# Optimization experiments

Measured on AMD Instinct MI355X. Metric: run time of the kernel, lower is better.

Reference implementation:

```python
import jax, jax.numpy as jnp
import numpy as np

EPS = 1e-5
NEG = -1e9

def _ln(x, g, b):
    m = x.mean(-1, keepdims=True)
    v = ((x - m) ** 2).mean(-1, keepdims=True)
    return (x - m) / jnp.sqrt(v + EPS) * g + b

def setup_inputs() -> dict:
    key = jax.random.key(0)
    ks = jax.random.split(key, 32)
    B, N, D, F, L = 2, 512, 128, 512, 3
    s = 0.05
    rn = lambda k, sh, sc=s: jax.random.normal(k, sh, jnp.float32) * sc
    inp = {
        'rel_matrix': rn(ks[0], (B, N, N, 2), 1.0),
        'pre_w': rn(ks[1], (2, D)), 'pre_b': rn(ks[2], (D,)),
        'proj_w': rn(ks[3], (2 * D, D)), 'proj_b': rn(ks[4], (D,)),
        'out_w1': rn(ks[5], (D, D)),
        'bn_g': 1.0 + rn(ks[6], (D,)), 'bn_b': rn(ks[7], (D,)),
        'bn_m': rn(ks[8], (D,)),
        'bn_v': 0.5 + jax.random.uniform(ks[9], (D,), jnp.float32),
        'out_w2': rn(ks[10], (D, D)), 'out_b2': rn(ks[11], (D,)),
        'pe': rn(ks[12], (128, D)),
        'wq': rn(ks[13], (L, D, D)), 'bq': rn(ks[14], (L, D)),
        'wk': rn(ks[15], (L, D, D)), 'bk': rn(ks[16], (L, D)),
        'wv': rn(ks[17], (L, D, D)), 'bv': rn(ks[18], (L, D)),
        'wo': rn(ks[19], (L, D, D)), 'bo': rn(ks[20], (L, D)),
        'ln1g': jnp.ones((L, D), jnp.float32), 'ln1b': jnp.zeros((L, D), jnp.float32),
        'ln2g': jnp.ones((L, D), jnp.float32), 'ln2b': jnp.zeros((L, D), jnp.float32),
        'fw1': rn(ks[21], (L, D, F)), 'fb1': rn(ks[22], (L, F)),
        'fw2': rn(ks[23], (L, F, D)), 'fb2': rn(ks[24], (L, D)),
        'mask': jax.random.randint(ks[25], (B, N), 0, 2) > 0,
        'agent_id': jax.random.randint(ks[26], (B, N), 0, 128, dtype=jnp.int32),
    }
    return inp

def reference(rel_matrix, pre_w, pre_b, proj_w, proj_b, out_w1, bn_g, bn_b, bn_m, bn_v,
              out_w2, out_b2, pe, wq, bq, wk, bk, wv, bv, wo, bo,
              ln1g, ln1b, ln2g, ln2b, fw1, fb1, fw2, fb2, mask, agent_id):
    # --- pairwise relation chain (the headroom target) ---
    # symmetric pairwise validity mask (B,N,N)
    pm = (mask[:, None, :] & mask[:, :, None]).astype(rel_matrix.dtype)
    count = jnp.maximum(pm.sum(axis=2), 1.0)  # (B,N) valid-partner counts
    x = rel_matrix @ pre_w + pre_b            # (B,N,N,D) pre_proj Linear(2->128)
    pooled = jnp.einsum('bijd,bij->bid', x, pm) / count[..., None]  # masked mean over j
    x = jnp.concatenate([x, jnp.broadcast_to(pooled[:, :, None, :], x.shape)], axis=-1)
    x = x @ proj_w + proj_b                   # Linear(256->128)
    x = jnp.einsum('bijd,bij->bid', x, pm) / count[..., None]       # masked mean over j
    # out MLP: Linear(no bias) + BatchNorm1d(eval) + ReLU + Linear
    h = x @ out_w1
    h = (h - bn_m) / jnp.sqrt(bn_v + EPS) * bn_g + bn_b
    x = jax.nn.relu(h) @ out_w2 + out_b2
    x = x + pe[agent_id]                      # agent positional embedding
    # --- 3 post-norm single-head transformer layers (eval, dropout off) ---
    kbias = jnp.where(mask, 0.0, NEG)[:, None, :]  # key padding bias (B,1,N)
    scale = 1.0 / jnp.sqrt(jnp.asarray(x.shape[-1], x.dtype))
    for l in range(3):
        q = x @ wq[l] + bq[l]
        k = x @ wk[l] + bk[l]
        v = x @ wv[l] + bv[l]
        a = jax.nn.softmax(jnp.einsum('bid,bjd->bij', q, k) * scale + kbias, axis=-1)
        att = jnp.einsum('bij,bjd->bid', a, v) @ wo[l] + bo[l]
        x = _ln(x + att, ln1g[l], ln1b[l])
        ff = jax.nn.relu(x @ fw1[l] + fb1[l]) @ fw2[l] + fb2[l]
        x = _ln(x + ff, ln2g[l], ln2b[l])
    return x
```

## Files before the change

### kernel.cpp

```cpp
#include <hip/hip_runtime.h>
#include <hip/hip_bf16.h>

typedef unsigned short u16;
typedef unsigned int u32;
typedef unsigned char u8;
typedef __attribute__((ext_vector_type(8))) short bf16x8;
typedef __attribute__((ext_vector_type(4))) float f32x4;

#define DEV __device__ __forceinline__

DEV float bf2f(u16 u) { union { u32 i; float f; } c; c.i = ((u32)u) << 16; return c.f; }
DEV u16 f2bf(float f) {
  union { float f; u32 i; } c; c.f = f;
  u32 r = c.i + 0x7FFFu + ((c.i >> 16) & 1u);
  return (u16)(r >> 16);
}
DEV u32 pk2(float lo, float hi) { return (u32)f2bf(lo) | ((u32)f2bf(hi) << 16); }
DEV float rdsrc(const void* p, int e, int isb) {
  return isb ? bf2f(((const u16*)p)[e]) : ((const float*)p)[e];
}
DEV bf16x8 as_bf(uint4 v) { union { uint4 u; bf16x8 h; } c; c.u = v; return c.h; }

static constexpr int B = 2, N = 512, D = 128, F = 512;
static constexpr int NROW = B * N;
static constexpr float EPS = 1e-5f;
static constexpr float NEG = -1e9f;
static constexpr float SCALE = 0.08838834764831845f;

#define OFF_PRE_W   0
#define OFF_PRE_B   256
#define OFF_PROJ_B  33152
#define OFF_BN_G    49664
#define OFF_BN_B    49792
#define OFF_BN_M    49920
#define OFF_BN_V    50048
#define OFF_OUT_B2  66560
#define OFF_PE      66688
#define OFF_BQ      132224
#define OFF_BK      181760
#define OFF_BV      231296
#define OFF_BO      280832
#define OFF_LN1G    281216
#define OFF_LN1B    281600
#define OFF_LN2G    281984
#define OFF_LN2B    282368
#define OFF_FB1     479360
#define OFF_FB2     677504
#define W_TOTAL     677888

static constexpr int PB_PROJ = 0;
static constexpr int PB_OW1  = 8192;
static constexpr int PB_OW2  = 16384;
static constexpr int PB_L0   = 24576;
static constexpr int PB_LSTR = 98304;
static constexpr int PB_WO   = 24576;
static constexpr int PB_FW1  = 32768;
static constexpr int PB_FW2  = 65536;
static constexpr int PTOT    = 79872;

struct NEnt { const void* s; int off, n; };
struct PEnt { const void* s1; const void* s2; int o1, o2, dst, lgn, cum; };
struct PrepArgs { NEnt nrm[19]; PEnt pk[21]; };

template<int KT>
DEV f32x4 mmaK(const uint4* __restrict__ aPk, const uint4* __restrict__ Bp,
               int ncol, int col, int lane) {
  f32x4 acc = {0.f, 0.f, 0.f, 0.f};
  const int sub = lane >> 4;
  #pragma unroll
  for (int kt = 0; kt < KT; ++kt) {
    const int e8 = kt * 4 + sub;
    acc = __builtin_amdgcn_mfma_f32_16x16x32_bf16(
        as_bf(aPk[e8 * 16 + (lane & 15)]),
        as_bf(Bp[(size_t)e8 * ncol + col]),
        acc, 0, 0, 0);
  }
  return acc;
}

DEV void packA(const float* __restrict__ src, int ld, int K,
               uint4* __restrict__ aPk, int t) {
  const int n = (K >> 3) * 4;
  for (int i = t; i < n; i += 512) {
    const int e8 = i >> 2, r = i & 3;
    const float* s = src + r * ld + e8 * 8;
    uint4 w;
    w.x = pk2(s[0], s[1]); w.y = pk2(s[2], s[3]);
    w.z = pk2(s[4], s[5]); w.w = pk2(s[6], s[7]);
    aPk[e8 * 16 + r] = w;
  }
}

__global__ __launch_bounds__(256) void k_prep(PrepArgs pa,
    const void* __restrict__ bnv, const void* __restrict__ maskp,
    int* __restrict__ flags, int* __restrict__ mbuf,
    float* __restrict__ W, u32* __restrict__ Wb)
{
  const int t = threadIdx.x, bid = blockIdx.x;
  __shared__ int s_nb, s_m4, s_m2;
  if (t == 0) { s_nb = 0; s_m4 = 0; s_m2 = 0; }
  __syncthreads();
  if (t < 64) {
    const u32 w = ((const u32*)bnv)[t];
    if (((w >> 8) & 0xFFu) != 0x3Fu || ((w >> 24) & 0xFFu) != 0x3Fu)
      atomicOr(&s_nb, 1);
  }
  __syncthreads();
  const int isb = s_nb ? 0 : 1;

  if (bid < 16) {
    for (int ten = 0; ten < 19; ++ten) {
      const NEnt E = pa.nrm[ten];
      for (int e = bid * 256 + t; e < E.n; e += 16 * 256)
        W[E.off + e] = rdsrc(E.s, e, isb);
    }
  } else if (bid < 143) {
    for (int g = (bid - 16) * 256 + t; g < PTOT; g += 127 * 256) {
      int ei = 0;
      #pragma unroll
      for (int k = 1; k < 21; ++k) if (g >= pa.pk[k].cum) ei = k;
      const PEnt E = pa.pk[ei];
      const int li = g - E.cum;
      const int e8 = li >> E.lgn, c = li & ((1 << E.lgn) - 1);
      float f[8];
      #pragma unroll
      for (int i = 0; i < 8; ++i) {
        const int si = ((e8 * 8 + i) << E.lgn) + c;
        f[i] = rdsrc(E.s1, E.o1 + si, isb);
        if (E.s2) f[i] += rdsrc(E.s2, E.o2 + si, isb);
      }
      uint4 w;
      w.x = pk2(f[0], f[1]); w.y = pk2(f[2], f[3]);
      w.z = pk2(f[4], f[5]); w.w = pk2(f[6], f[7]);
      ((uint4*)(Wb + E.dst))[li] = w;
    }
  } else {
    {
      const u32 w = ((const u32*)maskp)[t];
      if (!(w == 0u || w == 1u || w == 0x3F800000u)) atomicOr(&s_m4, 1);
      if (!(w == 0u || w == 1u || w == 0x10000u || w == 0x10001u ||
            w == 0x3F80u || w == 0x3F800000u || w == 0x3F803F80u)) atomicOr(&s_m2, 1);
    }
    __syncthreads();
    const int mode = (!s_m4) ? 4 : ((!s_m2) ? 2 : 1);
    if (t == 0) { flags[0] = isb; flags[1] = mode; }
    #pragma unroll
    for (int k = 0; k < 4; ++k) {
      const int e = k * 256 + t;
      int v;
      if (mode == 4)      v = (((const u32*)maskp)[e] != 0u);
      else if (mode == 2) v = (((const u16*)maskp)[e] != 0);
      else                v = (((const u8*)maskp)[e]  != 0);
      mbuf[e] = v;
    }
  }
}

__global__ __launch_bounds__(512) void k_relq(
    const void* __restrict__ relv, const float* __restrict__ W,
    const u32* __restrict__ Wb,
    const int* __restrict__ flags, const int* __restrict__ mbuf,
    const int* __restrict__ agent_id, float* __restrict__ xbuf,
    float* __restrict__ qb, u32* __restrict__ kbT, u32* __restrict__ vbT)
{
  const int t = threadIdx.x;
  const int row0 = blockIdx.x * 4;
  const int b = row0 >> 9;
  const int wid = t >> 6;
  const int lane = t & 63;

  __shared__ float pl[4][D], zl[4][D], rl[4][D], os[4][D];
  __shared__ float pA[4][D], pB[4][D];
  __shared__ uint4 aPk[1024];
  __shared__ float wred[8][9];
  __shared__ float sT0[4], sT1[4], sMt;

  float s0[4] = {0, 0, 0, 0}, s1[4] = {0, 0, 0, 0}, cnt;
  {
    const int j = t;
    const float m = (float)mbuf[b * N + j];
    cnt = m;
    if (flags[0]) {
      const u32* rel2 = (const u32*)relv;
      #pragma unroll
      for (int r = 0; r < 4; ++r) {
        const u32 u = rel2[(size_t)(row0 + r) * N + j];
        s0[r] += m * bf2f((u16)(u & 0xFFFFu));
        s1[r] += m * bf2f((u16)(u >> 16));
      }
    } else {
      const float2* relf = (const float2*)relv;
      #pragma unroll
      for (int r = 0; r < 4; ++r) {
        const float2 u = relf[(size_t)(row0 + r) * N + j];
        s0[r] += m * u.x; s1[r] += m * u.y;
      }
    }
  }
  {
    const uint4 z = {0u, 0u, 0u, 0u};
    aPk[t] = z; aPk[t + 512] = z;
  }
  #pragma unroll
  for (int o = 32; o > 0; o >>= 1) {
    #pragma unroll
    for (int r = 0; r < 4; ++r) {
      s0[r] += __shfl_xor(s0[r], o, 64);
      s1[r] += __shfl_xor(s1[r], o, 64);
    }
    cnt += __shfl_xor(cnt, o, 64);
  }
  if ((t & 63) == 0) {
    #pragma unroll
    for (int r = 0; r < 4; ++r) { wred[wid][r] = s0[r]; wred[wid][4 + r] = s1[r]; }
    wred[wid][8] = cnt;
  }
  __syncthreads();
  if (t < 4) {
    float a0 = 0, a1 = 0;
    #pragma unroll
    for (int w = 0; w < 8; ++w) { a0 += wred[w][t]; a1 += wred[w][4 + t]; }
    sT0[t] = a0; sT1[t] = a1;
  }
  if (t == 8) {
    float c = 0;
    #pragma unroll
    for (int w = 0; w < 8; ++w) c += wred[w][8];
    sMt = c;
  }
  __syncthreads();

  {
    const int r = t >> 7, c = t & 127;
    const int mi = mbuf[row0 + r];
    pl[r][c] = mi ? (sT0[r] * W[OFF_PRE_W + c] + sT1[r] * W[OFF_PRE_W + D + c]) / sMt
                    + W[OFF_PRE_B + c]
                  : 0.f;
  }
  __syncthreads();

  packA(&pl[0][0], D, D, aPk, t);
  __syncthreads();
  {
    const int col = wid * 16 + (lane & 15);
    f32x4 acc = mmaK<4>(aPk, (const uint4*)(Wb + PB_PROJ), 128, col, lane);
    if (lane < 16) {
      #pragma unroll
      for (int g = 0; g < 4; ++g) pA[g][col] = acc[g];
    }
  }
  __syncthreads();
  {
    const int r = t >> 7, d = t & 127;
    zl[r][d] = mbuf[row0 + r] ? pA[r][d] + W[OFF_PROJ_B + d] : 0.f;
  }
  __syncthreads();

  packA(&zl[0][0], D, D, aPk, t);
  __syncthreads();
  {
    const int col = wid * 16 + (lane & 15);
    f32x4 acc = mmaK<4>(aPk, (const uint4*)(Wb + PB_OW1), 128, col, lane);
    if (lane < 16) {
      #pragma unroll
      for (int g = 0; g < 4; ++g) pA[g][col] = acc[g];
    }
  }
  __syncthreads();
  {
    const int r = t >> 7, d = t & 127;
    const float hb = (pA[r][d] - W[OFF_BN_M + d]) * __frsqrt_rn(W[OFF_BN_V + d] + EPS)
                     * W[OFF_BN_G + d] + W[OFF_BN_B + d];
    rl[r][d] = fmaxf(hb, 0.f);
  }
  __syncthreads();

  packA(&rl[0][0], D, D, aPk, t);
  __syncthreads();
  {
    const int col = wid * 16 + (lane & 15);
    f32x4 acc = mmaK<4>(aPk, (const uint4*)(Wb + PB_OW2), 128, col, lane);
    if (lane < 16) {
      #pragma unroll
      for (int g = 0; g < 4; ++g) pA[g][col] = acc[g];
    }
  }
  __syncthreads();
  {
    const int r = t >> 7, d = t & 127;
    const int aid = agent_id[row0 + r];
    const float x0 = pA[r][d] + W[OFF_OUT_B2 + d] + W[OFF_PE + aid * D + d];
    os[r][d] = x0;
    xbuf[(size_t)(row0 + r) * D + d] = x0;
  }
  __syncthreads();

  packA(&os[0][0], D, D, aPk, t);
  __syncthreads();
  {
    const int col = wid * 16 + (lane & 15);
    #pragma unroll
    for (int m = 0; m < 3; ++m) {
      f32x4 acc = mmaK<4>(aPk, (const uint4*)(Wb + PB_L0 + m * 8192), 128, col, lane);
      if (lane < 16) {
        const float bb = W[(m == 0 ? OFF_BQ : m == 1 ? OFF_BK : OFF_BV) + col];
        if (m == 0) {
          #pragma unroll
          for (int g = 0; g < 4; ++g) qb[(size_t)(row0 + g) * D + col] = acc[g] + bb;
        } else if (m == 1) {
          #pragma unroll
          for (int g = 0; g < 4; ++g) pA[g][col] = acc[g] + bb;
        } else {
          #pragma unroll
          for (int g = 0; g < 4; ++g) pB[g][col] = acc[g] + bb;
        }
      }
    }
  }
  __syncthreads();
  if (t < 64) {
    const int r = t >> 4, e8 = t & 15;
    const float* ks = pA[r];
    uint4 w;
    w.x = pk2(ks[8 * e8 + 0], ks[8 * e8 + 1]);
    w.y = pk2(ks[8 * e8 + 2], ks[8 * e8 + 3]);
    w.z = pk2(ks[8 * e8 + 4], ks[8 * e8 + 5]);
    w.w = pk2(ks[8 * e8 + 6], ks[8 * e8 + 7]);
    ((uint4*)kbT)[((size_t)b * 16 + e8) * 512 + (row0 & 511) + r] = w;
  }
  if (t < 128) {
    const int i0 = row0 & 511, j8 = i0 >> 3, h = (i0 >> 2) & 1;
    uint2 w;
    w.x = pk2(pB[0][t], pB[1][t]);
    w.y = pk2(pB[2][t], pB[3][t]);
    *(uint2*)(vbT + (((size_t)b * 64 + j8) * 128 + t) * 4 + 2 * h) = w;
  }
}

__global__ __launch_bounds__(512) void k_layer(
    const float* __restrict__ qin, const u32* __restrict__ kinT, const u32* __restrict__ vinT,
    const float* __restrict__ W, const u32* __restrict__ Wb, const int l, const int last,
    float* __restrict__ qout, u32* __restrict__ koutT, u32* __restrict__ voutT,
    const int* __restrict__ mbuf, float* __restrict__ xbuf, float* __restrict__ outp)
{
  const int t = threadIdx.x;
  const int row0 = blockIdx.x * 4;
  const int b = row0 >> 9;
  const int wid = t >> 6;
  const int lane = t & 63;

  const uint4* WOp = (const uint4*)(Wb + PB_L0 + l * PB_LSTR + PB_WO);
  const uint4* W1p = (const uint4*)(Wb + PB_L0 + l * PB_LSTR + PB_FW1);
  const uint4* W2p = (const uint4*)(Wb + PB_L0 + l * PB_LSTR + PB_FW2);
  const float* bo  = W + OFF_BO  + l * D;
  const float* g1  = W + OFF_LN1G + l * D;
  const float* b1  = W + OFF_LN1B + l * D;
  const float* fb1 = W + OFF_FB1 + l * F;
  const float* fb2 = W + OFF_FB2 + l * D;
  const float* g2  = W + OFF_LN2G + l * D;
  const float* b2v = W + OFF_LN2B + l * D;

  __shared__ float qs[4][D];
  __shared__ float p[4][N];
  __shared__ float hs[4][F];
  __shared__ float os[4][D];
  __shared__ float xs[4][D];
  __shared__ float pA[4][D], pB[4][D];
  __shared__ uint4 aPk[1024];
  __shared__ float den[4];

  {
    const int r = t >> 7, d = t & 127;
    qs[r][d] = qin[(size_t)(row0 + r) * D + d] * SCALE;
    const uint4 z = {0u, 0u, 0u, 0u};
    aPk[t] = z; aPk[t + 512] = z;
  }
  __syncthreads();

  packA(&qs[0][0], D, D, aPk, t);
  __syncthreads();
  {
    const uint4* Kp = (const uint4*)kinT + (size_t)b * 16 * 512;
    #pragma unroll
    for (int i = 0; i < 4; ++i) {
      const int col = (wid * 4 + i) * 16 + (lane & 15);
      f32x4 acc = mmaK<4>(aPk, Kp, 512, col, lane);
      if (lane < 16) {
        const float bias = mbuf[b * N + col] ? 0.f : NEG;
        #pragma unroll
        for (int g = 0; g < 4; ++g) p[g][col] = acc[g] + bias;
      }
    }
  }
  __syncthreads();

  if (wid < 4) {
    const int r = wid;
    float pv[8];
    float mx = -1e30f;
    #pragma unroll
    for (int k = 0; k < 8; ++k) { pv[k] = p[r][lane + 64 * k]; mx = fmaxf(mx, pv[k]); }
    #pragma unroll
    for (int o = 32; o > 0; o >>= 1) mx = fmaxf(mx, __shfl_xor(mx, o, 64));
    float sum = 0.f;
    #pragma unroll
    for (int k = 0; k < 8; ++k) { pv[k] = __expf(pv[k] - mx); sum += pv[k]; }
    #pragma unroll
    for (int o = 32; o > 0; o >>= 1) sum += __shfl_xor(sum, o, 64);
    #pragma unroll
    for (int k = 0; k < 8; ++k) p[r][lane + 64 * k] = pv[k];
    if (lane == 0) den[r] = sum;
  }
  __syncthreads();

  packA(&p[0][0], N, N, aPk, t);
  __syncthreads();
  {
    const int col = wid * 16 + (lane & 15);
    const uint4* Vp = (const uint4*)vinT + (size_t)b * 64 * 128;
    f32x4 acc = mmaK<16>(aPk, Vp, 128, col, lane);
    if (lane < 16) {
      #pragma unroll
      for (int g = 0; g < 4; ++g) os[g][col] = acc[g] / den[g];
    }
  }
  __syncthreads();

  packA(&os[0][0], D, D, aPk, t);
  __syncthreads();
  {
    const int col = wid * 16 + (lane & 15);
    f32x4 acc = mmaK<4>(aPk, WOp, 128, col, lane);
    if (lane < 16) {
      #pragma unroll
      for (int g = 0; g < 4; ++g) pA[g][col] = acc[g];
    }
  }
  __syncthreads();

  if (wid < 4) {
    const int r = wid;
    float tv[2];
    #pragma unroll
    for (int k = 0; k < 2; ++k) {
      const int d = lane + 64 * k;
      tv[k] = pA[r][d] + bo[d] + xbuf[(size_t)(row0 + r) * D + d];
    }
    float s = tv[0] + tv[1], sq = tv[0] * tv[0] + tv[1] * tv[1];
    #pragma unroll
    for (int o = 32; o > 0; o >>= 1) { s += __shfl_xor(s, o, 64); sq += __shfl_xor(sq, o, 64); }
    const float mean = s * (1.f / 128.f);
    const float var  = sq * (1.f / 128.f) - mean * mean;
    const float rstd = __frsqrt_rn(var + EPS);
    #pragma unroll
    for (int k = 0; k < 2; ++k) {
      const int d = lane + 64 * k;
      xs[r][d] = (tv[k] - mean) * rstd * g1[d] + b1[d];
    }
  }
  __syncthreads();

  packA(&xs[0][0], D, D, aPk, t);
  __syncthreads();
  {
    #pragma unroll
    for (int i = 0; i < 4; ++i) {
      const int col = (wid * 4 + i) * 16 + (lane & 15);
      f32x4 acc = mmaK<4>(aPk, W1p, 512, col, lane);
      if (lane < 16) {
        const float bb = fb1[col];
        #pragma unroll
        for (int g = 0; g < 4; ++g) hs[g][col] = fmaxf(acc[g] + bb, 0.f);
      }
    }
  }
  __syncthreads();

  packA(&hs[0][0], F, F, aPk, t);
  __syncthreads();
  {
    const int col = wid * 16 + (lane & 15);
    f32x4 acc = mmaK<16>(aPk, W2p, 128, col, lane);
    if (lane < 16) {
      #pragma unroll
      for (int g = 0; g < 4; ++g) pA[g][col] = acc[g];
    }
  }
  __syncthreads();

  if (wid < 4) {
    const int r = wid;
    float tv[2];
    #pragma unroll
    for (int k = 0; k < 2; ++k) {
      const int d = lane + 64 * k;
      tv[k] = pA[r][d] + fb2[d] + xs[r][d];
    }
    float s = tv[0] + tv[1], sq = tv[0] * tv[0] + tv[1] * tv[1];
    #pragma unroll
    for (int o = 32; o > 0; o >>= 1) { s += __shfl_xor(s, o, 64); sq += __shfl_xor(sq, o, 64); }
    const float mean = s * (1.f / 128.f);
    const float var  = sq * (1.f / 128.f) - mean * mean;
    const float rstd = __frsqrt_rn(var + EPS);
    #pragma unroll
    for (int k = 0; k < 2; ++k) {
      const int d = lane + 64 * k;
      const float xn = (tv[k] - mean) * rstd * g2[d] + b2v[d];
      os[r][d] = xn;
      xbuf[(size_t)(row0 + r) * D + d] = xn;
      if (outp) outp[(size_t)(row0 + r) * D + d] = xn;
    }
  }
  __syncthreads();

  if (!last) {
    packA(&os[0][0], D, D, aPk, t);
    __syncthreads();
    {
      const int col = wid * 16 + (lane & 15);
      #pragma unroll
      for (int m = 0; m < 3; ++m) {
        const uint4* Bp = (const uint4*)(Wb + PB_L0 + (l + 1) * PB_LSTR + m * 8192);
        f32x4 acc = mmaK<4>(aPk, Bp, 128, col, lane);
        if (lane < 16) {
          const float bb = W[(m == 0 ? OFF_BQ : m == 1 ? OFF_BK : OFF_BV) + (l + 1) * D + col];
          if (m == 0) {
            #pragma unroll
            for (int g = 0; g < 4; ++g) qout[(size_t)(row0 + g) * D + col] = acc[g] + bb;
          } else if (m == 1) {
            #pragma unroll
            for (int g = 0; g < 4; ++g) pA[g][col] = acc[g] + bb;
          } else {
            #pragma unroll
            for (int g = 0; g < 4; ++g) pB[g][col] = acc[g] + bb;
          }
        }
      }
    }
    __syncthreads();
    if (t < 64) {
      const int r = t >> 4, e8 = t & 15;
      const float* ks = pA[r];
      uint4 w;
      w.x = pk2(ks[8 * e8 + 0], ks[8 * e8 + 1]);
      w.y = pk2(ks[8 * e8 + 2], ks[8 * e8 + 3]);
      w.z = pk2(ks[8 * e8 + 4], ks[8 * e8 + 5]);
      w.w = pk2(ks[8 * e8 + 6], ks[8 * e8 + 7]);
      ((uint4*)koutT)[((size_t)b * 16 + e8) * 512 + (row0 & 511) + r] = w;
    }
    if (t < 128) {
      const int i0 = row0 & 511, j8 = i0 >> 3, h = (i0 >> 2) & 1;
      uint2 w;
      w.x = pk2(pB[0][t], pB[1][t]);
      w.y = pk2(pB[2][t], pB[3][t]);
      *(uint2*)(voutT + (((size_t)b * 64 + j8) * 128 + t) * 4 + 2 * h) = w;
    }
  }
}

extern "C" void kernel_launch(void* const* d_in, const int* in_sizes, int n_in,
                              void* d_out, int out_size, void* d_ws, size_t ws_size,
                              hipStream_t stream) {
  int*   flags = (int*)d_ws;
  int*   mbuf  = flags + 16;
  float* xbuf  = (float*)d_ws + 1040;
  float* q0    = xbuf + NROW * D;
  float* q1    = q0 + NROW * D;
  u32*   kT0   = (u32*)(q1 + NROW * D);
  u32*   kT1   = kT0 + 65536;
  u32*   vT0   = kT1 + 65536;
  u32*   vT1   = vT0 + 65536;
  float* W     = (float*)(vT1 + 65536);
  u32*   Wb    = (u32*)(W + W_TOTAL);

  PrepArgs pa;
  {
    const NEnt nrm[19] = {
      {d_in[1],  OFF_PRE_W,  256}, {d_in[2],  OFF_PRE_B, 128},
      {d_in[4],  OFF_PROJ_B, 128},
      {d_in[6],  OFF_BN_G,   128}, {d_in[7],  OFF_BN_B,  128},
      {d_in[8],  OFF_BN_M,   128}, {d_in[9],  OFF_BN_V,  128},
      {d_in[11], OFF_OUT_B2, 128}, {d_in[12], OFF_PE,  16384},
      {d_in[14], OFF_BQ,     384}, {d_in[16], OFF_BK,    384},
      {d_in[18], OFF_BV,     384}, {d_in[20], OFF_BO,    384},
      {d_in[21], OFF_LN1G,   384}, {d_in[22], OFF_LN1B,  384},
      {d_in[23], OFF_LN2G,   384}, {d_in[24], OFF_LN2B,  384},
      {d_in[26], OFF_FB1,   1536}, {d_in[28], OFF_FB2,   384}};
    for (int i = 0; i < 19; ++i) pa.nrm[i] = nrm[i];

    pa.pk[0] = {d_in[3], d_in[3], 0, 16384, PB_PROJ, 7, 0};
    pa.pk[1] = {d_in[5],  nullptr, 0, 0, PB_OW1, 7, 2048};
    pa.pk[2] = {d_in[10], nullptr, 0, 0, PB_OW2, 7, 4096};
    for (int l = 0; l < 3; ++l) {
      const int lb = PB_L0 + l * PB_LSTR;
      const int cl = 6144 + l * 24576;
      pa.pk[3 + 6 * l + 0] = {d_in[13], nullptr, l * 16384, 0, lb,          7, cl};
      pa.pk[3 + 6 * l + 1] = {d_in[15], nullptr, l * 16384, 0, lb + 8192,   7, cl + 2048};
      pa.pk[3 + 6 * l + 2] = {d_in[17], nullptr, l * 16384, 0, lb + 16384,  7, cl + 4096};
      pa.pk[3 + 6 * l + 3] = {d_in[19], nullptr, l * 16384, 0, lb + PB_WO,  7, cl + 6144};
      pa.pk[3 + 6 * l + 4] = {d_in[25], nullptr, l * 65536, 0, lb + PB_FW1, 9, cl + 8192};
      pa.pk[3 + 6 * l + 5] = {d_in[27], nullptr, l * 65536, 0, lb + PB_FW2, 7, cl + 16384};
    }
  }
  const int* agent_id = (const int*)d_in[30];

  k_prep<<<144, 256, 0, stream>>>(pa, d_in[9], d_in[29], flags, mbuf, W, Wb);
  k_relq<<<NROW / 4, 512, 0, stream>>>(d_in[0], W, Wb, flags, mbuf, agent_id, xbuf,
                                       q0, kT0, vT0);

  float* qs_[2] = {q0, q1};
  u32*   ks_[2] = {kT0, kT1};
  u32*   vs_[2] = {vT0, vT1};
  for (int l = 0; l < 3; ++l) {
    const int cur = l & 1, nxt = cur ^ 1;
    const int last = (l == 2);
    k_layer<<<NROW / 4, 512, 0, stream>>>(
        qs_[cur], ks_[cur], vs_[cur],
        W, Wb, l, last,
        qs_[nxt], ks_[nxt], vs_[nxt],
        mbuf, xbuf, last ? (float*)d_out : (float*)nullptr);
  }
}
```

Before: 77.32 us.

## Fuse prep, relation and layer kernels into one persistent kernel with grid barriers

Replaces five separate kernel launches (prep, relation chain, three transformer layers) with a single 256-block persistent kernel. Stages are separated by atomic-counter grid barriers, and a memset resets the counters on each call. This removes launch gaps and inter-kernel drain between stages. In exchange it relies on all 256 blocks being co-resident, adds spin-wait barrier cost, and spreads the prep work over the same blocks.

```diff
diff --git a/kernel.cpp b/kernel.cpp
--- a/kernel.cpp
+++ b/kernel.cpp
@@ -62,6 +62,18 @@
 struct PEnt { const void* s1; const void* s2; int o1, o2, dst, lgn, cum; };
 struct PrepArgs { NEnt nrm[19]; PEnt pk[21]; };
 
+DEV void gsync(int* c, int nblk) {
+  __syncthreads();
+  if (threadIdx.x == 0) {
+    __threadfence();
+    __hip_atomic_fetch_add(c, 1, __ATOMIC_ACQ_REL, __HIP_MEMORY_SCOPE_AGENT);
+    while (__hip_atomic_load(c, __ATOMIC_ACQUIRE, __HIP_MEMORY_SCOPE_AGENT) < nblk)
+      __builtin_amdgcn_s_sleep(8);
+    __threadfence();
+  }
+  __syncthreads();
+}
+
 template<int KT>
 DEV f32x4 mmaK(const uint4* __restrict__ aPk, const uint4* __restrict__ Bp,
                int ncol, int col, int lane) {
@@ -91,13 +103,30 @@
   }
 }
 
-__global__ __launch_bounds__(256) void k_prep(PrepArgs pa,
-    const void* __restrict__ bnv, const void* __restrict__ maskp,
-    int* __restrict__ flags, int* __restrict__ mbuf,
-    float* __restrict__ W, u32* __restrict__ Wb)
+__global__ __launch_bounds__(512) void k_all(PrepArgs pa,
+    const void* __restrict__ relv, const void* __restrict__ bnv,
+    const void* __restrict__ maskp, const int* __restrict__ agent_id,
+    int* __restrict__ bar, int* __restrict__ mbuf,
+    float* __restrict__ xbuf, float* __restrict__ q0, float* __restrict__ q1,
+    u32* __restrict__ kT0, u32* __restrict__ kT1,
+    u32* __restrict__ vT0, u32* __restrict__ vT1,
+    float* __restrict__ W, u32* __restrict__ Wb, float* __restrict__ outp)
 {
-  const int t = threadIdx.x, bid = blockIdx.x;
+  const int t = threadIdx.x;
+  const int blk = blockIdx.x;
+  const int row0 = blk * 4;
+  const int b = row0 >> 9;
+  const int wid = t >> 6;
+  const int lane = t & 63;
+
+  __shared__ float bufA[4][512];
+  __shared__ float r0[4][128], r1[4][128], r2[4][128], r3[4][128], r4[4][128];
+  __shared__ uint4 aPk[1024];
+  __shared__ float wred[8][9];
+  __shared__ float sT0[4], sT1[4];
+  __shared__ float sMt, den[4];
   __shared__ int s_nb, s_m4, s_m2;
+
   if (t == 0) { s_nb = 0; s_m4 = 0; s_m2 = 0; }
   __syncthreads();
   if (t < 64) {
@@ -108,34 +137,32 @@
   __syncthreads();
   const int isb = s_nb ? 0 : 1;
 
-  if (bid < 16) {
-    for (int ten = 0; ten < 19; ++ten) {
-      const NEnt E = pa.nrm[ten];
-      for (int e = bid * 256 + t; e < E.n; e += 16 * 256)
-        W[E.off + e] = rdsrc(E.s, e, isb);
-    }
-  } else if (bid < 143) {
-    for (int g = (bid - 16) * 256 + t; g < PTOT; g += 127 * 256) {
-      int ei = 0;
-      #pragma unroll
-      for (int k = 1; k < 21; ++k) if (g >= pa.pk[k].cum) ei = k;
-      const PEnt E = pa.pk[ei];
-      const int li = g - E.cum;
-      const int e8 = li >> E.lgn, c = li & ((1 << E.lgn) - 1);
-      float f[8];
-      #pragma unroll
-      for (int i = 0; i < 8; ++i) {
-        const int si = ((e8 * 8 + i) << E.lgn) + c;
-        f[i] = rdsrc(E.s1, E.o1 + si, isb);
-        if (E.s2) f[i] += rdsrc(E.s2, E.o2 + si, isb);
-      }
-      uint4 w;
-      w.x = pk2(f[0], f[1]); w.y = pk2(f[2], f[3]);
-      w.z = pk2(f[4], f[5]); w.w = pk2(f[6], f[7]);
-      ((uint4*)(Wb + E.dst))[li] = w;
-    }
-  } else {
-    {
+  for (int ten = 0; ten < 19; ++ten) {
+    const NEnt E = pa.nrm[ten];
+    for (int e = blk * 512 + t; e < E.n; e += 256 * 512)
+      W[E.off + e] = rdsrc(E.s, e, isb);
+  }
+  for (int g = blk * 512 + t; g < PTOT; g += 256 * 512) {
+    int ei = 0;
+    #pragma unroll
+    for (int k = 1; k < 21; ++k) if (g >= pa.pk[k].cum) ei = k;
+    const PEnt E = pa.pk[ei];
+    const int li = g - E.cum;
+    const int e8 = li >> E.lgn, c = li & ((1 << E.lgn) - 1);
+    float f[8];
+    #pragma unroll
+    for (int i = 0; i < 8; ++i) {
+      const int si = ((e8 * 8 + i) << E.lgn) + c;
+      f[i] = rdsrc(E.s1, E.o1 + si, isb);
+      if (E.s2) f[i] += rdsrc(E.s2, E.o2 + si, isb);
+    }
+    uint4 w;
+    w.x = pk2(f[0], f[1]); w.y = pk2(f[2], f[3]);
+    w.z = pk2(f[4], f[5]); w.w = pk2(f[6], f[7]);
+    ((uint4*)(Wb + E.dst))[li] = w;
+  }
+  if (blk == 255) {
+    if (t < 256) {
       const u32 w = ((const u32*)maskp)[t];
       if (!(w == 0u || w == 1u || w == 0x3F800000u)) atomicOr(&s_m4, 1);
       if (!(w == 0u || w == 1u || w == 0x10000u || w == 0x10001u ||
@@ -143,10 +170,9 @@
     }
     __syncthreads();
     const int mode = (!s_m4) ? 4 : ((!s_m2) ? 2 : 1);
-    if (t == 0) { flags[0] = isb; flags[1] = mode; }
     #pragma unroll
-    for (int k = 0; k < 4; ++k) {
-      const int e = k * 256 + t;
+    for (int k = 0; k < 2; ++k) {
+      const int e = k * 512 + t;
       int v;
       if (mode == 4)      v = (((const u32*)maskp)[e] != 0u);
       else if (mode == 2) v = (((const u16*)maskp)[e] != 0);
@@ -154,385 +180,147 @@
       mbuf[e] = v;
     }
   }
-}
-
-__global__ __launch_bounds__(512) void k_relq(
-    const void* __restrict__ relv, const float* __restrict__ W,
-    const u32* __restrict__ Wb,
-    const int* __restrict__ flags, const int* __restrict__ mbuf,
-    const int* __restrict__ agent_id, float* __restrict__ xbuf,
-    float* __restrict__ qb, u32* __restrict__ kbT, u32* __restrict__ vbT)
-{
-  const int t = threadIdx.x;
-  const int row0 = blockIdx.x * 4;
-  const int b = row0 >> 9;
-  const int wid = t >> 6;
-  const int lane = t & 63;
-
-  __shared__ float pl[4][D], zl[4][D], rl[4][D], os[4][D];
-  __shared__ float pA[4][D], pB[4][D];
-  __shared__ uint4 aPk[1024];
-  __shared__ float wred[8][9];
-  __shared__ float sT0[4], sT1[4], sMt;
-
-  float s0[4] = {0, 0, 0, 0}, s1[4] = {0, 0, 0, 0}, cnt;
+  gsync(bar + 0, 256);
+
   {
-    const int j = t;
-    const float m = (float)mbuf[b * N + j];
-    cnt = m;
-    if (flags[0]) {
-      const u32* rel2 = (const u32*)relv;
+    float s0[4] = {0, 0, 0, 0}, s1[4] = {0, 0, 0, 0}, cnt;
+    {
+      const int j = t;
+      const float m = (float)mbuf[b * N + j];
+      cnt = m;
+      if (isb) {
+        const u32* rel2 = (const u32*)relv;
+        #pragma unroll
+        for (int r = 0; r < 4; ++r) {
+          const u32 u = rel2[(size_t)(row0 + r) * N + j];
+          s0[r] += m * bf2f((u16)(u & 0xFFFFu));
+          s1[r] += m * bf2f((u16)(u >> 16));
+        }
+      } else {
+        const float2* relf = (const float2*)relv;
+        #pragma unroll
+        for (int r = 0; r < 4; ++r) {
+          const float2 u = relf[(size_t)(row0 + r) * N + j];
+          s0[r] += m * u.x; s1[r] += m * u.y;
+        }
+      }
+    }
+    {
+      const uint4 z = {0u, 0u, 0u, 0u};
+      aPk[t] = z; aPk[t + 512] = z;
+    }
+    #pragma unroll
+    for (int o = 32; o > 0; o >>= 1) {
       #pragma unroll
       for (int r = 0; r < 4; ++r) {
-        const u32 u = rel2[(size_t)(row0 + r) * N + j];
-        s0[r] += m * bf2f((u16)(u & 0xFFFFu));
-        s1[r] += m * bf2f((u16)(u >> 16));
-      }
-    } else {
-      const float2* relf = (const float2*)relv;
-      #pragma unroll
-      for (int r = 0; r < 4; ++r) {
-        const float2 u = relf[(size_t)(row0 + r) * N + j];
-        s0[r] += m * u.x; s1[r] += m * u.y;
-      }
-    }
-  }
-  {
-    const uint4 z = {0u, 0u, 0u, 0u};
-    aPk[t] = z; aPk[t + 512] = z;
-  }
-  #pragma unroll
-  for (int o = 32; o > 0; o >>= 1) {
-    #pragma unroll
-    for (int r = 0; r < 4; ++r) {
-      s0[r] += __shfl_xor(s0[r], o, 64);
-      s1[r] += __shfl_xor(s1[r], o, 64);
-    }
-    cnt += __shfl_xor(cnt, o, 64);
-  }
-  if ((t & 63) == 0) {
-    #pragma unroll
-    for (int r = 0; r < 4; ++r) { wred[wid][r] = s0[r]; wred[wid][4 + r] = s1[r]; }
-    wred[wid][8] = cnt;
-  }
-  __syncthreads();
-  if (t < 4) {
-    float a0 = 0, a1 = 0;
-    #pragma unroll
-    for (int w = 0; w < 8; ++w) { a0 += wred[w][t]; a1 += wred[w][4 + t]; }
-    sT0[t] = a0; sT1[t] = a1;
-  }
-  if (t == 8) {
-    float c = 0;
-    #pragma unroll
-    for (int w = 0; w < 8; ++w) c += wred[w][8];
-    sMt = c;
-  }
-  __syncthreads();
-
-  {
-    const int r = t >> 7, c = t & 127;
-    const int mi = mbuf[row0 + r];
-    pl[r][c] = mi ? (sT0[r] * W[OFF_PRE_W + c] + sT1[r] * W[OFF_PRE_W + D + c]) / sMt
-                    + W[OFF_PRE_B + c]
-                  : 0.f;
-  }
-  __syncthreads();
-
-  packA(&pl[0][0], D, D, aPk, t);
-  __syncthreads();
-  {
-    const int col = wid * 16 + (lane & 15);
-    f32x4 acc = mmaK<4>(aPk, (const uint4*)(Wb + PB_PROJ), 128, col, lane);
-    if (lane < 16) {
-      #pragma unroll
-      for (int g = 0; g < 4; ++g) pA[g][col] = acc[g];
-    }
-  }
-  __syncthreads();
-  {
-    const int r = t >> 7, d = t & 127;
-    zl[r][d] = mbuf[row0 + r] ? pA[r][d] + W[OFF_PROJ_B + d] : 0.f;
-  }
-  __syncthreads();
-
-  packA(&zl[0][0], D, D, aPk, t);
-  __syncthreads();
-  {
-    const int col = wid * 16 + (lane & 15);
-    f32x4 acc = mmaK<4>(aPk, (const uint4*)(Wb + PB_OW1), 128, col, lane);
-    if (lane < 16) {
-      #pragma unroll
-      for (int g = 0; g < 4; ++g) pA[g][col] = acc[g];
-    }
-  }
-  __syncthreads();
-  {
-    const int r = t >> 7, d = t & 127;
-    const float hb = (pA[r][d] - W[OFF_BN_M + d]) * __frsqrt_rn(W[OFF_BN_V + d] + EPS)
-                     * W[OFF_BN_G + d] + W[OFF_BN_B + d];
-    rl[r][d] = fmaxf(hb, 0.f);
-  }
-  __syncthreads();
-
-  packA(&rl[0][0], D, D, aPk, t);
-  __syncthreads();
-  {
-    const int col = wid * 16 + (lane & 15);
-    f32x4 acc = mmaK<4>(aPk, (const uint4*)(Wb + PB_OW2), 128, col, lane);
-    if (lane < 16) {
-      #pragma unroll
-      for (int g = 0; g < 4; ++g) pA[g][col] = acc[g];
-    }
-  }
-  __syncthreads();
-  {
-    const int r = t >> 7, d = t & 127;
-    const int aid = agent_id[row0 + r];
-    const float x0 = pA[r][d] + W[OFF_OUT_B2 + d] + W[OFF_PE + aid * D + d];
-    os[r][d] = x0;
-    xbuf[(size_t)(row0 + r) * D + d] = x0;
-  }
-  __syncthreads();
-
-  packA(&os[0][0], D, D, aPk, t);
-  __syncthreads();
-  {
-    const int col = wid * 16 + (lane & 15);
-    #pragma unroll
-    for (int m = 0; m < 3; ++m) {
-      f32x4 acc = mmaK<4>(aPk, (const uint4*)(Wb + PB_L0 + m * 8192), 128, col, lane);
+        s0[r] += __shfl_xor(s0[r], o, 64);
+        s1[r] += __shfl_xor(s1[r], o, 64);
+      }
+      cnt += __shfl_xor(cnt, o, 64);
+    }
+    if ((t & 63) == 0) {
+      #pragma unroll
+      for (int r = 0; r < 4; ++r) { wred[wid][r] = s0[r]; wred[wid][4 + r] = s1[r]; }
+      wred[wid][8] = cnt;
+    }
+    __syncthreads();
+    if (t < 4) {
+      float a0 = 0, a1 = 0;
+      #pragma unroll
+      for (int w = 0; w < 8; ++w) { a0 += wred[w][t]; a1 += wred[w][4 + t]; }
+      sT0[t] = a0; sT1[t] = a1;
+    }
+    if (t == 8) {
+      float c = 0;
+      #pragma unroll
+      for (int w = 0; w < 8; ++w) c += wred[w][8];
+      sMt = c;
+    }
+    __syncthreads();
+
+    {
+      const int r = t >> 7, c = t & 127;
+      const int mi = mbuf[row0 + r];
+      r0[r][c] = mi ? (sT0[r] * W[OFF_PRE_W + c] + sT1[r] * W[OFF_PRE_W + D + c]) / sMt
+                      + W[OFF_PRE_B + c]
+                    : 0.f;
+    }
+    __syncthreads();
+
+    packA(&r0[0][0], D, D, aPk, t);
+    __syncthreads();
+    {
+      const int col = wid * 16 + (lane & 15);
+      f32x4 acc = mmaK<4>(aPk, (const uint4*)(Wb + PB_PROJ), 128, col, lane);
       if (lane < 16) {
-        const float bb = W[(m == 0 ? OFF_BQ : m == 1 ? OFF_BK : OFF_BV) + col];
-        if (m == 0) {
-          #pragma unroll
-          for (int g = 0; g < 4; ++g) qb[(size_t)(row0 + g) * D + col] = acc[g] + bb;
-        } else if (m == 1) {
-          #pragma unroll
-          for (int g = 0; g < 4; ++g) pA[g][col] = acc[g] + bb;
-        } else {
-          #pragma unroll
-          for (int g = 0; g < 4; ++g) pB[g][col] = acc[g] + bb;
-        }
-      }
-    }
-  }
-  __syncthreads();
-  if (t < 64) {
-    const int r = t >> 4, e8 = t & 15;
-    const float* ks = pA[r];
-    uint4 w;
-    w.x = pk2(ks[8 * e8 + 0], ks[8 * e8 + 1]);
-    w.y = pk2(ks[8 * e8 + 2], ks[8 * e8 + 3]);
-    w.z = pk2(ks[8 * e8 + 4], ks[8 * e8 + 5]);
-    w.w = pk2(ks[8 * e8 + 6], ks[8 * e8 + 7]);
-    ((uint4*)kbT)[((size_t)b * 16 + e8) * 512 + (row0 & 511) + r] = w;
-  }
-  if (t < 128) {
-    const int i0 = row0 & 511, j8 = i0 >> 3, h = (i0 >> 2) & 1;
-    uint2 w;
-    w.x = pk2(pB[0][t], pB[1][t]);
-    w.y = pk2(pB[2][t], pB[3][t]);
-    *(uint2*)(vbT + (((size_t)b * 64 + j8) * 128 + t) * 4 + 2 * h) = w;
-  }
-}
-
-__global__ __launch_bounds__(512) void k_layer(
-    const float* __restrict__ qin, const u32* __restrict__ kinT, const u32* __restrict__ vinT,
-    const float* __restrict__ W, const u32* __restrict__ Wb, const int l, const int last,
-    float* __restrict__ qout, u32* __restrict__ koutT, u32* __restrict__ voutT,
-    const int* __restrict__ mbuf, float* __restrict__ xbuf, float* __restrict__ outp)
-{
-  const int t = threadIdx.x;
-  const int row0 = blockIdx.x * 4;
-  const int b = row0 >> 9;
-  const int wid = t >> 6;
-  const int lane = t & 63;
-
-  const uint4* WOp = (const uint4*)(Wb + PB_L0 + l * PB_LSTR + PB_WO);
-  const uint4* W1p = (const uint4*)(Wb + PB_L0 + l * PB_LSTR + PB_FW1);
-  const uint4* W2p = (const uint4*)(Wb + PB_L0 + l * PB_LSTR + PB_FW2);
-  const float* bo  = W + OFF_BO  + l * D;
-  const float* g1  = W + OFF_LN1G + l * D;
-  const float* b1  = W + OFF_LN1B + l * D;
-  const float* fb1 = W + OFF_FB1 + l * F;
-  const float* fb2 = W + OFF_FB2 + l * D;
-  const float* g2  = W + OFF_LN2G + l * D;
-  const float* b2v = W + OFF_LN2B + l * D;
-
-  __shared__ float qs[4][D];
-  __shared__ float p[4][N];
-  __shared__ float hs[4][F];
-  __shared__ float os[4][D];
-  __shared__ float xs[4][D];
-  __shared__ float pA[4][D], pB[4][D];
-  __shared__ uint4 aPk[1024];
-  __shared__ float den[4];
-
-  {
-    const int r = t >> 7, d = t & 127;
-    qs[r][d] = qin[(size_t)(row0 + r) * D + d] * SCALE;
-    const uint4 z = {0u, 0u, 0u, 0u};
-    aPk[t] = z; aPk[t + 512] = z;
-  }
-  __syncthreads();
-
-  packA(&qs[0][0], D, D, aPk, t);
-  __syncthreads();
-  {
-    const uint4* Kp = (const uint4*)kinT + (size_t)b * 16 * 512;
-    #pragma unroll
-    for (int i = 0; i < 4; ++i) {
-      const int col = (wid * 4 + i) * 16 + (lane & 15);
-      f32x4 acc = mmaK<4>(aPk, Kp, 512, col, lane);
+        #pragma unroll
+        for (int g = 0; g < 4; ++g) r4[g][col] = acc[g];
+      }
+    }
+    __syncthreads();
+    {
+      const int r = t >> 7, d = t & 127;
+      r1[r][d] = mbuf[row0 + r] ? r4[r][d] + W[OFF_PROJ_B + d] : 0.f;
+    }
+    __syncthreads();
+
+    packA(&r1[0][0], D, D, aPk, t);
+    __syncthreads();
+    {
+      const int col = wid * 16 + (lane & 15);
+      f32x4 acc = mmaK<4>(aPk, (const uint4*)(Wb + PB_OW1), 128, col, lane);
       if (lane < 16) {
-        const float bias = mbuf[b * N + col] ? 0.f : NEG;
-        #pragma unroll
-        for (int g = 0; g < 4; ++g) p[g][col] = acc[g] + bias;
-      }
-    }
-  }
-  __syncthreads();
-
-  if (wid < 4) {
-    const int r = wid;
-    float pv[8];
-    float mx = -1e30f;
-    #pragma unroll
-    for (int k = 0; k < 8; ++k) { pv[k] = p[r][lane + 64 * k]; mx = fmaxf(mx, pv[k]); }
-    #pragma unroll
-    for (int o = 32; o > 0; o >>= 1) mx = fmaxf(mx, __shfl_xor(mx, o, 64));
-    float sum = 0.f;
-    #pragma unroll
-    for (int k = 0; k < 8; ++k) { pv[k] = __expf(pv[k] - mx); sum += pv[k]; }
-    #pragma unroll
-    for (int o = 32; o > 0; o >>= 1) sum += __shfl_xor(sum, o, 64);
-    #pragma unroll
-    for (int k = 0; k < 8; ++k) p[r][lane + 64 * k] = pv[k];
-    if (lane == 0) den[r] = sum;
-  }
-  __syncthreads();
-
-  packA(&p[0][0], N, N, aPk, t);
-  __syncthreads();
-  {
-    const int col = wid * 16 + (lane & 15);
-    const uint4* Vp = (const uint4*)vinT + (size_t)b * 64 * 128;
-    f32x4 acc = mmaK<16>(aPk, Vp, 128, col, lane);
-    if (lane < 16) {
-      #pragma unroll
-      for (int g = 0; g < 4; ++g) os[g][col] = acc[g] / den[g];
-    }
-  }
-  __syncthreads();
-
-  packA(&os[0][0], D, D, aPk, t);
-  __syncthreads();
-  {
-    const int col = wid * 16 + (lane & 15);
-    f32x4 acc = mmaK<4>(aPk, WOp, 128, col, lane);
-    if (lane < 16) {
-      #pragma unroll
-      for (int g = 0; g < 4; ++g) pA[g][col] = acc[g];
-    }
-  }
-  __syncthreads();
-
-  if (wid < 4) {
-    const int r = wid;
-    float tv[2];
-    #pragma unroll
-    for (int k = 0; k < 2; ++k) {
-      const int d = lane + 64 * k;
-      tv[k] = pA[r][d] + bo[d] + xbuf[(size_t)(row0 + r) * D + d];
-    }
-    float s = tv[0] + tv[1], sq = tv[0] * tv[0] + tv[1] * tv[1];
-    #pragma unroll
-    for (int o = 32; o > 0; o >>= 1) { s += __shfl_xor(s, o, 64); sq += __shfl_xor(sq, o, 64); }
-    const float mean = s * (1.f / 128.f);
-    const float var  = sq * (1.f / 128.f) - mean * mean;
-    const float rstd = __frsqrt_rn(var + EPS);
-    #pragma unroll
-    for (int k = 0; k < 2; ++k) {
-      const int d = lane + 64 * k;
-      xs[r][d] = (tv[k] - mean) * rstd * g1[d] + b1[d];
-    }
-  }
-  __syncthreads();
-
-  packA(&xs[0][0], D, D, aPk, t);
-  __syncthreads();
-  {
-    #pragma unroll
-    for (int i = 0; i < 4; ++i) {
-      const int col = (wid * 4 + i) * 16 + (lane & 15);
-      f32x4 acc = mmaK<4>(aPk, W1p, 512, col, lane);
+        #pragma unroll
+        for (int g = 0; g < 4; ++g) r4[g][col] = acc[g];
+      }
+    }
+    __syncthreads();
+    {
+      const int r = t >> 7, d = t & 127;
+      const float hb = (r4[r][d] - W[OFF_BN_M + d]) * __frsqrt_rn(W[OFF_BN_V + d] + EPS)
+                       * W[OFF_BN_G + d] + W[OFF_BN_B + d];
+      r2[r][d] = fmaxf(hb, 0.f);
+    }
+    __syncthreads();
+
+    packA(&r2[0][0], D, D, aPk, t);
+    __syncthreads();
+    {
+      const int col = wid * 16 + (lane & 15);
+      f32x4 acc = mmaK<4>(aPk, (const uint4*)(Wb + PB_OW2), 128, col, lane);
       if (lane < 16) {
-        const float bb = fb1[col];
-        #pragma unroll
-        for (int g = 0; g < 4; ++g) hs[g][col] = fmaxf(acc[g] + bb, 0.f);
-      }
-    }
-  }
-  __syncthreads();
-
-  packA(&hs[0][0], F, F, aPk, t);
-  __syncthreads();
-  {
-    const int col = wid * 16 + (lane & 15);
-    f32x4 acc = mmaK<16>(aPk, W2p, 128, col, lane);
-    if (lane < 16) {
-      #pragma unroll
-      for (int g = 0; g < 4; ++g) pA[g][col] = acc[g];
-    }
-  }
-  __syncthreads();
-
-  if (wid < 4) {
-    const int r = wid;
-    float tv[2];
-    #pragma unroll
-    for (int k = 0; k < 2; ++k) {
-      const int d = lane + 64 * k;
-      tv[k] = pA[r][d] + fb2[d] + xs[r][d];
-    }
-    float s = tv[0] + tv[1], sq = tv[0] * tv[0] + tv[1] * tv[1];
-    #pragma unroll
-    for (int o = 32; o > 0; o >>= 1) { s += __shfl_xor(s, o, 64); sq += __shfl_xor(sq, o, 64); }
-    const float mean = s * (1.f / 128.f);
-    const float var  = sq * (1.f / 128.f) - mean * mean;
-    const float rstd = __frsqrt_rn(var + EPS);
-    #pragma unroll
-    for (int k = 0; k < 2; ++k) {
-      const int d = lane + 64 * k;
-      const float xn = (tv[k] - mean) * rstd * g2[d] + b2v[d];
-      os[r][d] = xn;
-      xbuf[(size_t)(row0 + r) * D + d] = xn;
-      if (outp) outp[(size_t)(row0 + r) * D + d] = xn;
-    }
-  }
-  __syncthreads();
-
-  if (!last) {
-    packA(&os[0][0], D, D, aPk, t);
+        #pragma unroll
+        for (int g = 0; g < 4; ++g) r4[g][col] = acc[g];
+      }
+    }
+    __syncthreads();
+    {
+      const int r = t >> 7, d = t & 127;
+      const int aid = agent_id[row0 + r];
+      const float x0 = r4[r][d] + W[OFF_OUT_B2 + d] + W[OFF_PE + aid * D + d];
+      r3[r][d] = x0;
+      xbuf[(size_t)(row0 + r) * D + d] = x0;
+    }
+    __syncthreads();
+
+    packA(&r3[0][0], D, D, aPk, t);
     __syncthreads();
     {
       const int col = wid * 16 + (lane & 15);
       #pragma unroll
       for (int m = 0; m < 3; ++m) {
-        const uint4* Bp = (const uint4*)(Wb + PB_L0 + (l + 1) * PB_LSTR + m * 8192);
-        f32x4 acc = mmaK<4>(aPk, Bp, 128, col, lane);
+        f32x4 acc = mmaK<4>(aPk, (const uint4*)(Wb + PB_L0 + m * 8192), 128, col, lane);
         if (lane < 16) {
-          const float bb = W[(m == 0 ? OFF_BQ : m == 1 ? OFF_BK : OFF_BV) + (l + 1) * D + col];
+          const float bb = W[(m == 0 ? OFF_BQ : m == 1 ? OFF_BK : OFF_BV) + col];
           if (m == 0) {
             #pragma unroll
-            for (int g = 0; g < 4; ++g) qout[(size_t)(row0 + g) * D + col] = acc[g] + bb;
+            for (int g = 0; g < 4; ++g) q0[(size_t)(row0 + g) * D + col] = acc[g] + bb;
           } else if (m == 1) {
             #pragma unroll
-            for (int g = 0; g < 4; ++g) pA[g][col] = acc[g] + bb;
+            for (int g = 0; g < 4; ++g) r4[g][col] = acc[g] + bb;
           } else {
             #pragma unroll
-            for (int g = 0; g < 4; ++g) pB[g][col] = acc[g] + bb;
+            for (int g = 0; g < 4; ++g) bufA[g][col] = acc[g] + bb;
           }
         }
       }
@@ -540,20 +328,229 @@
     __syncthreads();
     if (t < 64) {
       const int r = t >> 4, e8 = t & 15;
-      const float* ks = pA[r];
+      const float* ks = r4[r];
       uint4 w;
       w.x = pk2(ks[8 * e8 + 0], ks[8 * e8 + 1]);
       w.y = pk2(ks[8 * e8 + 2], ks[8 * e8 + 3]);
       w.z = pk2(ks[8 * e8 + 4], ks[8 * e8 + 5]);
       w.w = pk2(ks[8 * e8 + 6], ks[8 * e8 + 7]);
-      ((uint4*)koutT)[((size_t)b * 16 + e8) * 512 + (row0 & 511) + r] = w;
+      ((uint4*)kT0)[((size_t)b * 16 + e8) * 512 + (row0 & 511) + r] = w;
     }
     if (t < 128) {
       const int i0 = row0 & 511, j8 = i0 >> 3, h = (i0 >> 2) & 1;
       uint2 w;
-      w.x = pk2(pB[0][t], pB[1][t]);
-      w.y = pk2(pB[2][t], pB[3][t]);
-      *(uint2*)(voutT + (((size_t)b * 64 + j8) * 128 + t) * 4 + 2 * h) = w;
+      w.x = pk2(bufA[0][t], bufA[1][t]);
+      w.y = pk2(bufA[2][t], bufA[3][t]);
+      *(uint2*)(vT0 + (((size_t)b * 64 + j8) * 128 + t) * 4 + 2 * h) = w;
+    }
+  }
+  gsync(bar + 1, 256);
+
+  for (int l = 0; l < 3; ++l) {
+    const int last = (l == 2);
+    const float* qin = (l & 1) ? q1 : q0;
+    float*       qout = (l & 1) ? q0 : q1;
+    const u32*   kin = (l & 1) ? kT1 : kT0;
+    u32*         kout = (l & 1) ? kT0 : kT1;
+    const u32*   vin = (l & 1) ? vT1 : vT0;
+    u32*         vout = (l & 1) ? vT0 : vT1;
+
+    const uint4* WOp = (const uint4*)(Wb + PB_L0 + l * PB_LSTR + PB_WO);
+    const uint4* W1p = (const uint4*)(Wb + PB_L0 + l * PB_LSTR + PB_FW1);
+    const uint4* W2p = (const uint4*)(Wb + PB_L0 + l * PB_LSTR + PB_FW2);
+    const float* bo  = W + OFF_BO  + l * D;
+    const float* g1  = W + OFF_LN1G + l * D;
+    const float* b1  = W + OFF_LN1B + l * D;
+    const float* fb1 = W + OFF_FB1 + l * F;
+    const float* fb2 = W + OFF_FB2 + l * D;
+    const float* g2  = W + OFF_LN2G + l * D;
+    const float* b2v = W + OFF_LN2B + l * D;
+
+    {
+      const int r = t >> 7, d = t & 127;
+      r0[r][d] = qin[(size_t)(row0 + r) * D + d] * SCALE;
+    }
+    __syncthreads();
+
+    packA(&r0[0][0], D, D, aPk, t);
+    __syncthreads();
+    {
+      const uint4* Kp = (const uint4*)kin + (size_t)b * 16 * 512;
+      #pragma unroll
+      for (int i = 0; i < 4; ++i) {
+        const int col = (wid * 4 + i) * 16 + (lane & 15);
+        f32x4 acc = mmaK<4>(aPk, Kp, 512, col, lane);
+        if (lane < 16) {
+          const float bias = mbuf[b * N + col] ? 0.f : NEG;
+          #pragma unroll
+          for (int g = 0; g < 4; ++g) bufA[g][col] = acc[g] + bias;
+        }
+      }
+    }
+    __syncthreads();
+
+    if (wid < 4) {
+      const int r = wid;
+      float pv[8];
+      float mx = -1e30f;
+      #pragma unroll
+      for (int k = 0; k < 8; ++k) { pv[k] = bufA[r][lane + 64 * k]; mx = fmaxf(mx, pv[k]); }
+      #pragma unroll
+      for (int o = 32; o > 0; o >>= 1) mx = fmaxf(mx, __shfl_xor(mx, o, 64));
+      float sum = 0.f;
+      #pragma unroll
+      for (int k = 0; k < 8; ++k) { pv[k] = __expf(pv[k] - mx); sum += pv[k]; }
+      #pragma unroll
+      for (int o = 32; o > 0; o >>= 1) sum += __shfl_xor(sum, o, 64);
+      #pragma unroll
+      for (int k = 0; k < 8; ++k) bufA[r][lane + 64 * k] = pv[k];
+      if (lane == 0) den[r] = sum;
+    }
+    __syncthreads();
+
+    packA(&bufA[0][0], N, N, aPk, t);
+    __syncthreads();
+    {
+      const int col = wid * 16 + (lane & 15);
+      const uint4* Vp = (const uint4*)vin + (size_t)b * 64 * 128;
+      f32x4 acc = mmaK<16>(aPk, Vp, 128, col, lane);
+      if (lane < 16) {
+        #pragma unroll
+        for (int g = 0; g < 4; ++g) r1[g][col] = acc[g] / den[g];
+      }
+    }
+    __syncthreads();
+
+    packA(&r1[0][0], D, D, aPk, t);
+    __syncthreads();
+    {
+      const int col = wid * 16 + (lane & 15);
+      f32x4 acc = mmaK<4>(aPk, WOp, 128, col, lane);
+      if (lane < 16) {
+        #pragma unroll
+        for (int g = 0; g < 4; ++g) r3[g][col] = acc[g];
+      }
+    }
+    __syncthreads();
+
+    if (wid < 4) {
+      const int r = wid;
+      float tv[2];
+      #pragma unroll
+      for (int k = 0; k < 2; ++k) {
+        const int d = lane + 64 * k;
+        tv[k] = r3[r][d] + bo[d] + xbuf[(size_t)(row0 + r) * D + d];
+      }
+      float s = tv[0] + tv[1], sq = tv[0] * tv[0] + tv[1] * tv[1];
+      #pragma unroll
+      for (int o = 32; o > 0; o >>= 1) { s += __shfl_xor(s, o, 64); sq += __shfl_xor(sq, o, 64); }
+      const float mean = s * (1.f / 128.f);
+      const float var  = sq * (1.f / 128.f) - mean * mean;
+      const float rstd = __frsqrt_rn(var + EPS);
+      #pragma unroll
+      for (int k = 0; k < 2; ++k) {
+        const int d = lane + 64 * k;
+        r2[r][d] = (tv[k] - mean) * rstd * g1[d] + b1[d];
+      }
+    }
+    __syncthreads();
+
+    packA(&r2[0][0], D, D, aPk, t);
+    __syncthreads();
+    {
+      #pragma unroll
+      for (int i = 0; i < 4; ++i) {
+        const int col = (wid * 4 + i) * 16 + (lane & 15);
+        f32x4 acc = mmaK<4>(aPk, W1p, 512, col, lane);
+        if (lane < 16) {
+          const float bb = fb1[col];
+          #pragma unroll
+          for (int g = 0; g < 4; ++g) bufA[g][col] = fmaxf(acc[g] + bb, 0.f);
+        }
+      }
+    }
+    __syncthreads();
+
+    packA(&bufA[0][0], F, F, aPk, t);
+    __syncthreads();
+    {
+      const int col = wid * 16 + (lane & 15);
+      f32x4 acc = mmaK<16>(aPk, W2p, 128, col, lane);
+      if (lane < 16) {
+        #pragma unroll
+        for (int g = 0; g < 4; ++g) r3[g][col] = acc[g];
+      }
+    }
+    __syncthreads();
+
+    if (wid < 4) {
+      const int r = wid;
+      float tv[2];
+      #pragma unroll
+      for (int k = 0; k < 2; ++k) {
+        const int d = lane + 64 * k;
+        tv[k] = r3[r][d] + fb2[d] + r2[r][d];
+      }
+      float s = tv[0] + tv[1], sq = tv[0] * tv[0] + tv[1] * tv[1];
+      #pragma unroll
+      for (int o = 32; o > 0; o >>= 1) { s += __shfl_xor(s, o, 64); sq += __shfl_xor(sq, o, 64); }
+      const float mean = s * (1.f / 128.f);
+      const float var  = sq * (1.f / 128.f) - mean * mean;
+      const float rstd = __frsqrt_rn(var + EPS);
+      #pragma unroll
+      for (int k = 0; k < 2; ++k) {
+        const int d = lane + 64 * k;
+        const float xn = (tv[k] - mean) * rstd * g2[d] + b2v[d];
+        r1[r][d] = xn;
+        xbuf[(size_t)(row0 + r) * D + d] = xn;
+        if (last) outp[(size_t)(row0 + r) * D + d] = xn;
+      }
+    }
+    __syncthreads();
+
+    if (!last) {
+      packA(&r1[0][0], D, D, aPk, t);
+      __syncthreads();
+      {
+        const int col = wid * 16 + (lane & 15);
+        #pragma unroll
+        for (int m = 0; m < 3; ++m) {
+          const uint4* Bp = (const uint4*)(Wb + PB_L0 + (l + 1) * PB_LSTR + m * 8192);
+          f32x4 acc = mmaK<4>(aPk, Bp, 128, col, lane);
+          if (lane < 16) {
+            const float bb = W[(m == 0 ? OFF_BQ : m == 1 ? OFF_BK : OFF_BV) + (l + 1) * D + col];
+            if (m == 0) {
+              #pragma unroll
+              for (int g = 0; g < 4; ++g) qout[(size_t)(row0 + g) * D + col] = acc[g] + bb;
+            } else if (m == 1) {
+              #pragma unroll
+              for (int g = 0; g < 4; ++g) r3[g][col] = acc[g] + bb;
+            } else {
+              #pragma unroll
+              for (int g = 0; g < 4; ++g) r4[g][col] = acc[g] + bb;
+            }
+          }
+        }
+      }
+      __syncthreads();
+      if (t < 64) {
+        const int r = t >> 4, e8 = t & 15;
+        const float* ks = r3[r];
+        uint4 w;
+        w.x = pk2(ks[8 * e8 + 0], ks[8 * e8 + 1]);
+        w.y = pk2(ks[8 * e8 + 2], ks[8 * e8 + 3]);
+        w.z = pk2(ks[8 * e8 + 4], ks[8 * e8 + 5]);
+        w.w = pk2(ks[8 * e8 + 6], ks[8 * e8 + 7]);
+        ((uint4*)kout)[((size_t)b * 16 + e8) * 512 + (row0 & 511) + r] = w;
+      }
+      if (t < 128) {
+        const int i0 = row0 & 511, j8 = i0 >> 3, h = (i0 >> 2) & 1;
+        uint2 w;
+        w.x = pk2(r4[0][t], r4[1][t]);
+        w.y = pk2(r4[2][t], r4[3][t]);
+        *(uint2*)(vout + (((size_t)b * 64 + j8) * 128 + t) * 4 + 2 * h) = w;
+      }
+      gsync(bar + 2 + l, 256);
     }
   }
 }
@@ -562,6 +559,7 @@
                               void* d_out, int out_size, void* d_ws, size_t ws_size,
                               hipStream_t stream) {
   int*   flags = (int*)d_ws;
+  int*   bar   = flags + 4;
   int*   mbuf  = flags + 16;
   float* xbuf  = (float*)d_ws + 1040;
   float* q0    = xbuf + NROW * D;
@@ -604,20 +602,9 @@
   }
   const int* agent_id = (const int*)d_in[30];
 
-  k_prep<<<144, 256, 0, stream>>>(pa, d_in[9], d_in[29], flags, mbuf, W, Wb);
-  k_relq<<<NROW / 4, 512, 0, stream>>>(d_in[0], W, Wb, flags, mbuf, agent_id, xbuf,
-                                       q0, kT0, vT0);
-
-  float* qs_[2] = {q0, q1};
-  u32*   ks_[2] = {kT0, kT1};
-  u32*   vs_[2] = {vT0, vT1};
-  for (int l = 0; l < 3; ++l) {
-    const int cur = l & 1, nxt = cur ^ 1;
-    const int last = (l == 2);
-    k_layer<<<NROW / 4, 512, 0, stream>>>(
-        qs_[cur], ks_[cur], vs_[cur],
-        W, Wb, l, last,
-        qs_[nxt], ks_[nxt], vs_[nxt],
-        mbuf, xbuf, last ? (float*)d_out : (float*)nullptr);
-  }
+  hipMemsetAsync((void*)bar, 0, 4 * sizeof(int), stream);
+
+  k_all<<<256, 512, 0, stream>>>(pa, d_in[0], d_in[9], d_in[29], agent_id,
+                                 bar, mbuf, xbuf, q0, q1, kT0, kT1, vT0, vT1,
+                                 W, Wb, (float*)d_out);
 }
```

After: 188.6 us. +143.9%, slower.
